# Optimization experiments

Hardware: AMD Instinct MI355X
Metric: run time of the kernel (lower is better)

## Reference

```python
import jax, jax.numpy as jnp
import numpy as np

N_ENC, IN_DIM, LATENT = 16, 256, 32
WIDTHS = [128, 64]
BATCH = 32768
NID_C = N_ENC * LATENT  # 512, identity width of the compressor


def _halving_widths():
    # halving_widths(n_encoders, 1) * n_encoders from the source
    ws, w = [], N_ENC
    while w >= 1:
        ws.append(N_ENC * w)
        w //= 2
    return ws  # [256, 128, 64, 32, 16]


def _residual_pairs(init_dim, final_dim):
    # (in, out) shapes of the linear layers inside the residual compressor/decompressor
    pairs, inp = [], 2 * init_dim  # DoublingBlock doubles the input first
    for o in _halving_widths():
        pairs.append((inp, o))
        inp = init_dim + o  # ResidualBlock output = identity (init_dim) + activated out
    pairs.append((inp, final_dim))
    return pairs


def setup_inputs() -> dict:
    key = jax.random.key(0)
    ks = iter(jax.random.split(key, 80))
    d = {}
    d["x"] = jax.random.normal(next(ks), (BATCH, N_ENC * IN_DIM), dtype=jnp.float32)
    enc_dims = [IN_DIM] + WIDTHS + [LATENT]
    for i in range(3):
        fi, fo = enc_dims[i], enc_dims[i + 1]
        d[f"enc_w{i}"] = jax.random.normal(next(ks), (N_ENC, fo, fi), dtype=jnp.float32) / np.float32(np.sqrt(fi))
        d[f"enc_b{i}"] = jnp.zeros((N_ENC, fo), dtype=jnp.float32)
    dec_dims = [LATENT] + WIDTHS[::-1] + [IN_DIM]
    for i in range(3):
        fi, fo = dec_dims[i], dec_dims[i + 1]
        d[f"dec_w{i}"] = jax.random.normal(next(ks), (N_ENC, fo, fi), dtype=jnp.float32) / np.float32(np.sqrt(fi))
        d[f"dec_b{i}"] = jnp.zeros((N_ENC, fo), dtype=jnp.float32)
    for i, (fi, fo) in enumerate(_residual_pairs(NID_C, LATENT)):
        d[f"comp_w{i}"] = jax.random.normal(next(ks), (fo, fi), dtype=jnp.float32) / np.float32(np.sqrt(fi))
        d[f"comp_b{i}"] = jnp.zeros((fo,), dtype=jnp.float32)
    for i, (fi, fo) in enumerate(_residual_pairs(LATENT, NID_C)):
        d[f"decomp_w{i}"] = jax.random.normal(next(ks), (fo, fi), dtype=jnp.float32) / np.float32(np.sqrt(fi))
        d[f"decomp_b{i}"] = jnp.zeros((fo,), dtype=jnp.float32)
    return d


def _stacked_mlp(h, ws, bs):
    # Block-diagonal stacked MLP: equivalent math to a dense Linear whose weight
    # is diagnolize_weights(per-model weights), expressed as a batched GEMM.
    B = h.shape[0]
    for i, (w, b) in enumerate(zip(ws, bs)):
        n, o, fi = w.shape
        h = jnp.einsum('bni,noi->bno', h.reshape(B, n, fi), w) + b  # b: (n, o)
        h = h.reshape(B, n * o)
        if i < len(ws) - 1:
            h = jax.nn.sigmoid(h)
    return h


def _residual_net(z, ws, bs, n_id):
    h = jnp.concatenate([z, z], axis=1)  # DoublingBlock
    for w, b in zip(ws[:-1], bs[:-1]):
        # ResidualBlock: concat(identity, act(Linear(full)))
        h = jnp.concatenate([h[:, :n_id], jax.nn.sigmoid(h @ w.T + b)], axis=1)
    return h @ ws[-1].T + bs[-1]


def reference(x, enc_w0, enc_b0, enc_w1, enc_b1, enc_w2, enc_b2,
              dec_w0, dec_b0, dec_w1, dec_b1, dec_w2, dec_b2,
              comp_w0, comp_b0, comp_w1, comp_b1, comp_w2, comp_b2,
              comp_w3, comp_b3, comp_w4, comp_b4, comp_w5, comp_b5,
              decomp_w0, decomp_b0, decomp_w1, decomp_b1, decomp_w2, decomp_b2,
              decomp_w3, decomp_b3, decomp_w4, decomp_b4, decomp_w5, decomp_b5):
    enc_ws = [enc_w0, enc_w1, enc_w2]; enc_bs = [enc_b0, enc_b1, enc_b2]
    dec_ws = [dec_w0, dec_w1, dec_w2]; dec_bs = [dec_b0, dec_b1, dec_b2]
    comp_ws = [comp_w0, comp_w1, comp_w2, comp_w3, comp_w4, comp_w5]
    comp_bs = [comp_b0, comp_b1, comp_b2, comp_b3, comp_b4, comp_b5]
    decomp_ws = [decomp_w0, decomp_w1, decomp_w2, decomp_w3, decomp_w4, decomp_w5]
    decomp_bs = [decomp_b0, decomp_b1, decomp_b2, decomp_b3, decomp_b4, decomp_b5]
    z_stack = _stacked_mlp(x, enc_ws, enc_bs)                 # (B, 512)
    z = _residual_net(z_stack, comp_ws, comp_bs, NID_C)       # (B, 32)
    z_stack_hat = _residual_net(z, decomp_ws, decomp_bs, LATENT)  # (B, 512)
    x_hat = _stacked_mlp(z_stack_hat, dec_ws, dec_bs)         # (B, 4096)
    return x_hat
```

## Files before the change

kernel.cpp:

```cpp
#include <hip/hip_runtime.h>

typedef __bf16 bf16x8 __attribute__((ext_vector_type(8)));
typedef __bf16 bf16x4 __attribute__((ext_vector_type(4)));
typedef float  f32x4  __attribute__((ext_vector_type(4)));

#define MFMA16(a, b, c) __builtin_amdgcn_mfma_f32_16x16x32_bf16((a), (b), (c), 0, 0, 0)

__device__ __forceinline__ float sigm(float x) { return 1.0f / (1.0f + __expf(-x)); }

enum : int {
  ENC_W0_OFF  = 0,
  ENC_W1_OFF  = 524288,
  ENC_W2_OFF  = 655360,
  DEC_W0_OFF  = 688128,
  DEC_W1_OFF  = 720896,
  DEC_W2_OFF  = 851968,
  COMP_W0_OFF = 1376256,
  COMP_W1_OFF = 1507328,
  COMP_W2_OFF = 1605632,
  COMP_W3_OFF = 1646592,
  COMP_W4_OFF = 1665024,
  COMP_W5_OFF = 1673728,
  DCMP_W0_OFF = 1691136,
  DCMP_W1_OFF = 1699328,
  DCMP_W2_OFF = 1736192,
  DCMP_W3_OFF = 1746432,
  DCMP_W4_OFF = 1749504,
  DCMP_W5_OFF = 1750528,
  W_TOTAL     = 1783296,
};

#define ZS_BYTES_OFF (4u * 1024u * 1024u)

__device__ __forceinline__ bf16x8 ldB(const __bf16* __restrict__ Wp, int nc16, int kf, int c, int lane) {
  return *(const bf16x8*)(Wp + (((size_t)(kf * nc16 + c)) * 64 + lane) * 8);
}

struct RC { int row, col; };
__device__ __forceinline__ RC unperm(int tl, int lg_nc16) {
  int frag = tl >> 9, ln = (tl >> 3) & 63, j = tl & 7;
  int kf = frag >> lg_nc16, c = frag & ((1 << lg_nc16) - 1);
  RC rc; rc.row = c * 16 + (ln & 15); rc.col = kf * 32 + ((ln >> 4) << 3) + j;
  return rc;
}

__global__ void prep_kernel(
    const float* __restrict__ ew0, const float* __restrict__ ew1, const float* __restrict__ ew2,
    const float* __restrict__ dw0, const float* __restrict__ dw1, const float* __restrict__ dw2,
    const float* __restrict__ cw0, const float* __restrict__ cw1, const float* __restrict__ cw2,
    const float* __restrict__ cw3, const float* __restrict__ cw4, const float* __restrict__ cw5,
    const float* __restrict__ xw0, const float* __restrict__ xw1, const float* __restrict__ xw2,
    const float* __restrict__ xw3, const float* __restrict__ xw4, const float* __restrict__ xw5,
    __bf16* __restrict__ wb)
{
  for (int i = blockIdx.x * blockDim.x + threadIdx.x; i < W_TOTAL; i += gridDim.x * blockDim.x) {
    float v;
    if (i < ENC_W1_OFF) {
      int t = i; int e = t >> 15; RC rc = unperm(t & 32767, 3);
      v = ew0[e * 32768 + rc.row * 256 + rc.col];
    } else if (i < ENC_W2_OFF) {
      int t = i - ENC_W1_OFF; int e = t >> 13; RC rc = unperm(t & 8191, 2);
      v = ew1[e * 8192 + rc.row * 128 + rc.col];
    } else if (i < DEC_W0_OFF) {
      int t = i - ENC_W2_OFF; int e = t >> 11; RC rc = unperm(t & 2047, 1);
      v = ew2[e * 2048 + rc.row * 64 + rc.col];
    } else if (i < DEC_W1_OFF) {
      int t = i - DEC_W0_OFF; int e = t >> 11; RC rc = unperm(t & 2047, 2);
      v = dw0[e * 2048 + rc.row * 32 + rc.col];
    } else if (i < DEC_W2_OFF) {
      int t = i - DEC_W1_OFF; int e = t >> 13; RC rc = unperm(t & 8191, 3);
      v = dw1[e * 8192 + rc.row * 64 + rc.col];
    } else if (i < COMP_W0_OFF) {
      int t = i - DEC_W2_OFF; int e = t >> 15; RC rc = unperm(t & 32767, 4);
      v = dw2[e * 32768 + rc.row * 128 + rc.col];
    } else if (i < COMP_W1_OFF) {
      RC rc = unperm(i - COMP_W0_OFF, 4);
      v = cw0[rc.row * 1024 + rc.col] + cw0[rc.row * 1024 + 512 + rc.col];
    } else if (i < COMP_W2_OFF) {
      RC rc = unperm(i - COMP_W1_OFF, 3); v = cw1[rc.row * 768 + rc.col];
    } else if (i < COMP_W3_OFF) {
      RC rc = unperm(i - COMP_W2_OFF, 2); v = cw2[rc.row * 640 + rc.col];
    } else if (i < COMP_W4_OFF) {
      RC rc = unperm(i - COMP_W3_OFF, 1); v = cw3[rc.row * 576 + rc.col];
    } else if (i < COMP_W5_OFF) {
      RC rc = unperm(i - COMP_W4_OFF, 0); v = cw4[rc.row * 544 + rc.col];
    } else if (i < DCMP_W0_OFF) {
      RC rc = unperm(i - COMP_W5_OFF, 1);
      v = (rc.col < 528) ? cw5[rc.row * 528 + rc.col] : 0.0f;
    } else if (i < DCMP_W1_OFF) {
      RC rc = unperm(i - DCMP_W0_OFF, 4);
      v = xw0[rc.row * 64 + rc.col] + xw0[rc.row * 64 + 32 + rc.col];
    } else if (i < DCMP_W2_OFF) {
      RC rc = unperm(i - DCMP_W1_OFF, 3); v = xw1[rc.row * 288 + rc.col];
    } else if (i < DCMP_W3_OFF) {
      RC rc = unperm(i - DCMP_W2_OFF, 2); v = xw2[rc.row * 160 + rc.col];
    } else if (i < DCMP_W4_OFF) {
      RC rc = unperm(i - DCMP_W3_OFF, 1); v = xw3[rc.row * 96 + rc.col];
    } else if (i < DCMP_W5_OFF) {
      RC rc = unperm(i - DCMP_W4_OFF, 0); v = xw4[rc.row * 64 + rc.col];
    } else {
      RC rc = unperm(i - DCMP_W5_OFF, 5);
      v = (rc.col < 48) ? xw5[rc.row * 48 + rc.col] : 0.0f;
    }
    wb[i] = (__bf16)v;
  }
}

__global__ __launch_bounds__(256, 3)
void enc_kernel(const float* __restrict__ x, const __bf16* __restrict__ wb,
                const float* __restrict__ b0, const float* __restrict__ b1,
                const float* __restrict__ b2, __bf16* __restrict__ zout)
{
  __shared__ __align__(16) char smem[51200];
  __bf16* xs = (__bf16*)smem;
  __bf16* h1 = (__bf16*)(smem + 33792);
  __bf16* h2 = (__bf16*)smem;
  const int e = blockIdx.x;
  const int m0 = blockIdx.y * 64;
  const int tid = threadIdx.x;
  const int lane = tid & 63, wv = tid >> 6;
  const int l15 = lane & 15, hi8 = (lane >> 4) * 8, rloc = (lane >> 4) * 4;

  const float* xblk = x + (size_t)m0 * 4096 + e * 256;
  #pragma unroll
  for (int i = 0; i < 16; ++i) {
    int idx = tid + i * 256;
    int r = idx >> 6, c4 = (idx & 63) * 4;
    float4 v = *(const float4*)(xblk + (size_t)r * 4096 + c4);
    bf16x4 o = { (__bf16)v.x, (__bf16)v.y, (__bf16)v.z, (__bf16)v.w };
    *(bf16x4*)&xs[r * 264 + c4] = o;
  }
  __syncthreads();

  {
    const __bf16* W = wb + ENC_W0_OFF + e * 32768;
    f32x4 acc[4][2];
    #pragma unroll
    for (int cf = 0; cf < 2; ++cf) {
      float bv = b0[e * 128 + wv * 32 + cf * 16 + l15];
      f32x4 bvv = {bv, bv, bv, bv};
      #pragma unroll
      for (int rf = 0; rf < 4; ++rf) acc[rf][cf] = bvv;
    }
    #pragma unroll
    for (int ks = 0; ks < 8; ++ks) {
      bf16x8 a[4], bb[2];
      #pragma unroll
      for (int rf = 0; rf < 4; ++rf) a[rf] = *(const bf16x8*)&xs[(rf * 16 + l15) * 264 + ks * 32 + hi8];
      #pragma unroll
      for (int cf = 0; cf < 2; ++cf) bb[cf] = ldB(W, 8, ks, wv * 2 + cf, lane);
      #pragma unroll
      for (int rf = 0; rf < 4; ++rf)
        #pragma unroll
        for (int cf = 0; cf < 2; ++cf)
          acc[rf][cf] = MFMA16(a[rf], bb[cf], acc[rf][cf]);
    }
    #pragma unroll
    for (int rf = 0; rf < 4; ++rf)
      #pragma unroll
      for (int cf = 0; cf < 2; ++cf)
        #pragma unroll
        for (int r = 0; r < 4; ++r)
          h1[(rf * 16 + rloc + r) * 136 + wv * 32 + cf * 16 + l15] = (__bf16)sigm(acc[rf][cf][r]);
  }
  __syncthreads();

  {
    const __bf16* W = wb + ENC_W1_OFF + e * 8192;
    f32x4 acc[4];
    float bv = b1[e * 64 + wv * 16 + l15];
    f32x4 bvv = {bv, bv, bv, bv};
    #pragma unroll
    for (int rf = 0; rf < 4; ++rf) acc[rf] = bvv;
    #pragma unroll
    for (int ks = 0; ks < 4; ++ks) {
      bf16x8 a[4];
      #pragma unroll
      for (int rf = 0; rf < 4; ++rf) a[rf] = *(const bf16x8*)&h1[(rf * 16 + l15) * 136 + ks * 32 + hi8];
      bf16x8 bb = ldB(W, 4, ks, wv, lane);
      #pragma unroll
      for (int rf = 0; rf < 4; ++rf) acc[rf] = MFMA16(a[rf], bb, acc[rf]);
    }
    #pragma unroll
    for (int rf = 0; rf < 4; ++rf)
      #pragma unroll
      for (int r = 0; r < 4; ++r)
        h2[(rf * 16 + rloc + r) * 72 + wv * 16 + l15] = (__bf16)sigm(acc[rf][r]);
  }
  __syncthreads();

  if (wv < 2) {
    const __bf16* W = wb + ENC_W2_OFF + e * 2048;
    f32x4 acc[4];
    float bv = b2[e * 32 + wv * 16 + l15];
    f32x4 bvv = {bv, bv, bv, bv};
    #pragma unroll
    for (int rf = 0; rf < 4; ++rf) acc[rf] = bvv;
    #pragma unroll
    for (int ks = 0; ks < 2; ++ks) {
      bf16x8 a[4];
      #pragma unroll
      for (int rf = 0; rf < 4; ++rf) a[rf] = *(const bf16x8*)&h2[(rf * 16 + l15) * 72 + ks * 32 + hi8];
      bf16x8 bb = ldB(W, 2, ks, wv, lane);
      #pragma unroll
      for (int rf = 0; rf < 4; ++rf) acc[rf] = MFMA16(a[rf], bb, acc[rf]);
    }
    #pragma unroll
    for (int rf = 0; rf < 4; ++rf)
      #pragma unroll
      for (int r = 0; r < 4; ++r)
        zout[(size_t)(m0 + rf * 16 + rloc + r) * 512 + e * 32 + wv * 16 + l15] = (__bf16)acc[rf][r];
  }
}

template<int NF, int KT, int ZKS, int ZLD, int SKS, int SLD, int DLD, bool SIG>
__device__ __forceinline__ void rlayer(const __bf16* __restrict__ W, const float* __restrict__ bias,
                                       const __bf16* __restrict__ zp, const __bf16* __restrict__ sp,
                                       __bf16* __restrict__ dst,
                                       int wv, int lane, int l15, int hi8, int rloc)
{
  constexpr int NJ = (NF >= 32) ? 4 : ((NF >= 16) ? 2 : 1);
  constexpr int NR = (NF >= 8) ? 4 : ((NF == 4) ? 2 : 1);
  int c0, row0;
  if constexpr (NF >= 8)       { c0 = wv;      row0 = 0; }
  else if constexpr (NF == 4)  { c0 = wv & 3;  row0 = (wv >> 2) * 32; }
  else if constexpr (NF == 2)  { c0 = wv & 1;  row0 = (wv >> 1) * 16; }
  else                         { if (wv >= 4) return; c0 = 0; row0 = wv * 16; }
  f32x4 acc[NR][NJ];
  #pragma unroll
  for (int j = 0; j < NJ; ++j) {
    float bv = bias[(c0 + 8 * j) * 16 + l15];
    f32x4 b4 = {bv, bv, bv, bv};
    #pragma unroll
    for (int rf = 0; rf < NR; ++rf) acc[rf][j] = b4;
  }
  #pragma unroll
  for (int ks = 0; ks < ZKS; ++ks) {
    bf16x8 a[NR];
    #pragma unroll
    for (int rf = 0; rf < NR; ++rf)
      a[rf] = *(const bf16x8*)&zp[(size_t)(row0 + rf * 16 + l15) * ZLD + ks * 32 + hi8];
    #pragma unroll
    for (int j = 0; j < NJ; ++j) {
      bf16x8 b = ldB(W, NF, ks, c0 + 8 * j, lane);
      #pragma unroll
      for (int rf = 0; rf < NR; ++rf) acc[rf][j] = MFMA16(a[rf], b, acc[rf][j]);
    }
  }
  if constexpr (SKS > 0) {
    #pragma unroll
    for (int ks = 0; ks < SKS; ++ks) {
      bf16x8 a[NR];
      #pragma unroll
      for (int rf = 0; rf < NR; ++rf)
        a[rf] = *(const bf16x8*)&sp[(size_t)(row0 + rf * 16 + l15) * SLD + ks * 32 + hi8];
      #pragma unroll
      for (int j = 0; j < NJ; ++j) {
        bf16x8 b = ldB(W, NF, ZKS + ks, c0 + 8 * j, lane);
        #pragma unroll
        for (int rf = 0; rf < NR; ++rf) acc[rf][j] = MFMA16(a[rf], b, acc[rf][j]);
      }
    }
  }
  #pragma unroll
  for (int j = 0; j < NJ; ++j)
    #pragma unroll
    for (int rf = 0; rf < NR; ++rf)
      #pragma unroll
      for (int r = 0; r < 4; ++r) {
        float v = acc[rf][j][r];
        dst[(size_t)(row0 + rf * 16 + rloc + r) * DLD + (c0 + 8 * j) * 16 + l15] =
            (__bf16)(SIG ? sigm(v) : v);
      }
}

struct MidBias {
  const float *c0, *c1, *c2, *c3, *c4, *c5;
  const float *x0, *x1, *x2, *x3, *x4, *x5;
};

__global__ __launch_bounds__(512, 2)
void mid_kernel(const __bf16* __restrict__ zin, const __bf16* __restrict__ wb,
                MidBias mb, __bf16* __restrict__ zhout)
{
  __shared__ __bf16 zs[64 * 520];
  __shared__ __bf16 sA[64 * 264];
  __shared__ __bf16 sB[64 * 136];
  __shared__ __bf16 zsm[64 * 40];
  const int tid = threadIdx.x;
  const int wv = tid >> 6, lane = tid & 63;
  const int l15 = lane & 15, hi8 = (lane >> 4) * 8, rloc = (lane >> 4) * 4;
  const int m0 = blockIdx.x * 64;

  #pragma unroll
  for (int i = 0; i < 8; ++i) {
    int idx = tid + i * 512;
    int r = idx >> 6, c8 = (idx & 63) * 8;
    *(bf16x8*)&zs[r * 520 + c8] = *(const bf16x8*)(zin + (size_t)(m0 + r) * 512 + c8);
  }
  __syncthreads();
  rlayer<16, 512, 16, 520, 0,   0, 264, true >(wb + COMP_W0_OFF, mb.c0, zs, nullptr, sA, wv, lane, l15, hi8, rloc); __syncthreads();
  rlayer< 8, 768, 16, 520, 8, 264, 136, true >(wb + COMP_W1_OFF, mb.c1, zs, sA, sB, wv, lane, l15, hi8, rloc); __syncthreads();
  rlayer< 4, 640, 16, 520, 4, 136, 264, true >(wb + COMP_W2_OFF, mb.c2, zs, sB, sA, wv, lane, l15, hi8, rloc); __syncthreads();
  rlayer< 2, 576, 16, 520, 2, 264, 136, true >(wb + COMP_W3_OFF, mb.c3, zs, sA, sB, wv, lane, l15, hi8, rloc); __syncthreads();
  rlayer< 1, 544, 16, 520, 1, 136, 264, true >(wb + COMP_W4_OFF, mb.c4, zs, sB, sA, wv, lane, l15, hi8, rloc);
  for (int i = tid; i < 64 * 16; i += 512) sA[(i >> 4) * 264 + 16 + (i & 15)] = (__bf16)0.0f;
  __syncthreads();
  rlayer< 2, 544, 16, 520, 1, 264, 40, false>(wb + COMP_W5_OFF, mb.c5, zs, sA, zsm, wv, lane, l15, hi8, rloc);
  __syncthreads();
  rlayer<16,  32, 1, 40, 0,   0, 264, true >(wb + DCMP_W0_OFF, mb.x0, zsm, nullptr, sA, wv, lane, l15, hi8, rloc); __syncthreads();
  rlayer< 8, 288, 1, 40, 8, 264, 136, true >(wb + DCMP_W1_OFF, mb.x1, zsm, sA, sB, wv, lane, l15, hi8, rloc); __syncthreads();
  rlayer< 4, 160, 1, 40, 4, 136, 264, true >(wb + DCMP_W2_OFF, mb.x2, zsm, sB, sA, wv, lane, l15, hi8, rloc); __syncthreads();
  rlayer< 2,  96, 1, 40, 2, 264, 136, true >(wb + DCMP_W3_OFF, mb.x3, zsm, sA, sB, wv, lane, l15, hi8, rloc); __syncthreads();
  rlayer< 1,  64, 1, 40, 1, 136, 264, true >(wb + DCMP_W4_OFF, mb.x4, zsm, sB, sA, wv, lane, l15, hi8, rloc);
  for (int i = tid; i < 64 * 16; i += 512) sA[(i >> 4) * 264 + 16 + (i & 15)] = (__bf16)0.0f;
  __syncthreads();
  rlayer<32,  64, 1, 40, 1, 264, 512, false>(wb + DCMP_W5_OFF, mb.x5, zsm, sA,
                                             zhout + (size_t)m0 * 512, wv, lane, l15, hi8, rloc);
}

__global__ __launch_bounds__(256, 4)
void dec_kernel(const __bf16* __restrict__ zin, const __bf16* __restrict__ wb,
                const float* __restrict__ b0, const float* __restrict__ b1,
                const float* __restrict__ b2, float* __restrict__ out)
{
  __shared__ __bf16 zs[64][40];
  __shared__ __bf16 h1[64][72];
  __shared__ __bf16 h2[64][136];
  const int e = blockIdx.x;
  const int m0 = blockIdx.y * 64;
  const int tid = threadIdx.x;
  const int lane = tid & 63, wv = tid >> 6;
  const int l15 = lane & 15, hi8 = (lane >> 4) * 8, rloc = (lane >> 4) * 4;

  {
    int r = tid >> 2, c = (tid & 3) * 8;
    *(bf16x8*)&zs[r][c] = *(const bf16x8*)(zin + (size_t)(m0 + r) * 512 + e * 32 + c);
  }
  __syncthreads();

  {
    const __bf16* W = wb + DEC_W0_OFF + e * 2048;
    f32x4 acc[4];
    float bv = b0[e * 64 + wv * 16 + l15];
    f32x4 bvv = {bv, bv, bv, bv};
    #pragma unroll
    for (int rf = 0; rf < 4; ++rf) acc[rf] = bvv;
    bf16x8 a[4];
    #pragma unroll
    for (int rf = 0; rf < 4; ++rf) a[rf] = *(const bf16x8*)&zs[rf * 16 + l15][hi8];
    bf16x8 bb = ldB(W, 4, 0, wv, lane);
    #pragma unroll
    for (int rf = 0; rf < 4; ++rf) acc[rf] = MFMA16(a[rf], bb, acc[rf]);
    #pragma unroll
    for (int rf = 0; rf < 4; ++rf)
      #pragma unroll
      for (int r = 0; r < 4; ++r)
        h1[rf * 16 + rloc + r][wv * 16 + l15] = (__bf16)sigm(acc[rf][r]);
  }
  __syncthreads();

  {
    const __bf16* W = wb + DEC_W1_OFF + e * 8192;
    f32x4 acc[4][2];
    #pragma unroll
    for (int cf = 0; cf < 2; ++cf) {
      float bv = b1[e * 128 + wv * 32 + cf * 16 + l15];
      f32x4 bvv = {bv, bv, bv, bv};
      #pragma unroll
      for (int rf = 0; rf < 4; ++rf) acc[rf][cf] = bvv;
    }
    #pragma unroll
    for (int ks = 0; ks < 2; ++ks) {
      bf16x8 a[4], bb[2];
      #pragma unroll
      for (int rf = 0; rf < 4; ++rf) a[rf] = *(const bf16x8*)&h1[rf * 16 + l15][ks * 32 + hi8];
      #pragma unroll
      for (int cf = 0; cf < 2; ++cf) bb[cf] = ldB(W, 8, ks, wv * 2 + cf, lane);
      #pragma unroll
      for (int rf = 0; rf < 4; ++rf)
        #pragma unroll
        for (int cf = 0; cf < 2; ++cf)
          acc[rf][cf] = MFMA16(a[rf], bb[cf], acc[rf][cf]);
    }
    #pragma unroll
    for (int rf = 0; rf < 4; ++rf)
      #pragma unroll
      for (int cf = 0; cf < 2; ++cf)
        #pragma unroll
        for (int r = 0; r < 4; ++r)
          h2[rf * 16 + rloc + r][wv * 32 + cf * 16 + l15] = (__bf16)sigm(acc[rf][cf][r]);
  }
  __syncthreads();

  {
    const __bf16* W = wb + DEC_W2_OFF + e * 32768;
    f32x4 acc[4][4];
    #pragma unroll
    for (int cf = 0; cf < 4; ++cf) {
      float bv = b2[e * 256 + wv * 64 + cf * 16 + l15];
      f32x4 bvv = {bv, bv, bv, bv};
      #pragma unroll
      for (int rf = 0; rf < 4; ++rf) acc[rf][cf] = bvv;
    }
    #pragma unroll
    for (int ks = 0; ks < 4; ++ks) {
      bf16x8 a[4], bb[4];
      #pragma unroll
      for (int rf = 0; rf < 4; ++rf) a[rf] = *(const bf16x8*)&h2[rf * 16 + l15][ks * 32 + hi8];
      #pragma unroll
      for (int cf = 0; cf < 4; ++cf) bb[cf] = ldB(W, 16, ks, wv * 4 + cf, lane);
      #pragma unroll
      for (int rf = 0; rf < 4; ++rf)
        #pragma unroll
        for (int cf = 0; cf < 4; ++cf)
          acc[rf][cf] = MFMA16(a[rf], bb[cf], acc[rf][cf]);
    }
    #pragma unroll
    for (int rf = 0; rf < 4; ++rf)
      #pragma unroll
      for (int cf = 0; cf < 4; ++cf)
        #pragma unroll
        for (int r = 0; r < 4; ++r)
          out[(size_t)(m0 + rf * 16 + rloc + r) * 4096 + e * 256 + wv * 64 + cf * 16 + l15] =
              acc[rf][cf][r];
  }
}

extern "C" void kernel_launch(void* const* d_in, const int* in_sizes, int n_in,
                              void* d_out, int out_size, void* d_ws, size_t ws_size,
                              hipStream_t stream) {
  (void)in_sizes; (void)n_in; (void)out_size; (void)ws_size;
  const float* x   = (const float*)d_in[0];
  const float* ew0 = (const float*)d_in[1];  const float* eb0 = (const float*)d_in[2];
  const float* ew1 = (const float*)d_in[3];  const float* eb1 = (const float*)d_in[4];
  const float* ew2 = (const float*)d_in[5];  const float* eb2 = (const float*)d_in[6];
  const float* dw0 = (const float*)d_in[7];  const float* db0 = (const float*)d_in[8];
  const float* dw1 = (const float*)d_in[9];  const float* db1 = (const float*)d_in[10];
  const float* dw2 = (const float*)d_in[11]; const float* db2 = (const float*)d_in[12];
  const float* cw[6]; const float* cb[6];
  for (int i = 0; i < 6; ++i) { cw[i] = (const float*)d_in[13 + 2 * i]; cb[i] = (const float*)d_in[14 + 2 * i]; }
  const float* xw[6]; const float* xb[6];
  for (int i = 0; i < 6; ++i) { xw[i] = (const float*)d_in[25 + 2 * i]; xb[i] = (const float*)d_in[26 + 2 * i]; }

  __bf16* wbuf   = (__bf16*)d_ws;
  __bf16* zstack = (__bf16*)((char*)d_ws + ZS_BYTES_OFF);
  float* out = (float*)d_out;

  prep_kernel<<<1024, 256, 0, stream>>>(ew0, ew1, ew2, dw0, dw1, dw2,
                                        cw[0], cw[1], cw[2], cw[3], cw[4], cw[5],
                                        xw[0], xw[1], xw[2], xw[3], xw[4], xw[5], wbuf);
  enc_kernel<<<dim3(16, 512), 256, 0, stream>>>(x, wbuf, eb0, eb1, eb2, zstack);
  MidBias mb = {cb[0], cb[1], cb[2], cb[3], cb[4], cb[5],
                xb[0], xb[1], xb[2], xb[3], xb[4], xb[5]};
  mid_kernel<<<512, 512, 0, stream>>>(zstack, wbuf, mb, zstack);
  dec_kernel<<<dim3(16, 512), 256, 0, stream>>>(zstack, wbuf, db0, db1, db2, out);
}
```

Baseline: 345.3 us.

## Double encoder block to 512 threads and redistribute MFMA tiles across eight waves

The encoder kernel now launches 512 threads per block instead of 256, with launch bounds raised to allow up to six blocks per CU. Each of the eight waves takes a narrower slice of every layer: one 16-column fragment in layer 0, a 16x32 sub-tile in layer 1, and a single 16x16 tile in layer 2, so all waves stay busy in the last layer where half of them were idle before. The aim is more latency hiding and better use of the CU during the memory-heavy x load. In exchange each wave gets less register reuse of the A fragments, LDS read traffic per MFMA goes up, and the tighter launch bounds may cap registers per thread.

```diff
diff --git a/kernel.cpp b/kernel.cpp
--- a/kernel.cpp
+++ b/kernel.cpp
@@ -106,7 +106,7 @@
   }
 }
 
-__global__ __launch_bounds__(256, 3)
+__global__ __launch_bounds__(512, 6)
 void enc_kernel(const float* __restrict__ x, const __bf16* __restrict__ wb,
                 const float* __restrict__ b0, const float* __restrict__ b1,
                 const float* __restrict__ b2, __bf16* __restrict__ zout)
@@ -123,8 +123,8 @@
 
   const float* xblk = x + (size_t)m0 * 4096 + e * 256;
   #pragma unroll
-  for (int i = 0; i < 16; ++i) {
-    int idx = tid + i * 256;
+  for (int i = 0; i < 8; ++i) {
+    int idx = tid + i * 512;
     int r = idx >> 6, c4 = (idx & 63) * 4;
     float4 v = *(const float4*)(xblk + (size_t)r * 4096 + c4);
     bf16x4 o = { (__bf16)v.x, (__bf16)v.y, (__bf16)v.z, (__bf16)v.w };
@@ -134,82 +134,66 @@
 
   {
     const __bf16* W = wb + ENC_W0_OFF + e * 32768;
-    f32x4 acc[4][2];
-    #pragma unroll
-    for (int cf = 0; cf < 2; ++cf) {
-      float bv = b0[e * 128 + wv * 32 + cf * 16 + l15];
-      f32x4 bvv = {bv, bv, bv, bv};
-      #pragma unroll
-      for (int rf = 0; rf < 4; ++rf) acc[rf][cf] = bvv;
-    }
+    f32x4 acc[4];
+    float bv = b0[e * 128 + wv * 16 + l15];
+    f32x4 bvv = {bv, bv, bv, bv};
+    #pragma unroll
+    for (int rf = 0; rf < 4; ++rf) acc[rf] = bvv;
     #pragma unroll
     for (int ks = 0; ks < 8; ++ks) {
-      bf16x8 a[4], bb[2];
-      #pragma unroll
-      for (int rf = 0; rf < 4; ++rf) a[rf] = *(const bf16x8*)&xs[(rf * 16 + l15) * 264 + ks * 32 + hi8];
-      #pragma unroll
-      for (int cf = 0; cf < 2; ++cf) bb[cf] = ldB(W, 8, ks, wv * 2 + cf, lane);
-      #pragma unroll
-      for (int rf = 0; rf < 4; ++rf)
-        #pragma unroll
-        for (int cf = 0; cf < 2; ++cf)
-          acc[rf][cf] = MFMA16(a[rf], bb[cf], acc[rf][cf]);
+      bf16x8 bb = ldB(W, 8, ks, wv, lane);
+      #pragma unroll
+      for (int rf = 0; rf < 4; ++rf) {
+        bf16x8 a = *(const bf16x8*)&xs[(rf * 16 + l15) * 264 + ks * 32 + hi8];
+        acc[rf] = MFMA16(a, bb, acc[rf]);
+      }
     }
     #pragma unroll
     for (int rf = 0; rf < 4; ++rf)
       #pragma unroll
-      for (int cf = 0; cf < 2; ++cf)
-        #pragma unroll
-        for (int r = 0; r < 4; ++r)
-          h1[(rf * 16 + rloc + r) * 136 + wv * 32 + cf * 16 + l15] = (__bf16)sigm(acc[rf][cf][r]);
+      for (int r = 0; r < 4; ++r)
+        h1[(rf * 16 + rloc + r) * 136 + wv * 16 + l15] = (__bf16)sigm(acc[rf][r]);
   }
   __syncthreads();
 
   {
     const __bf16* W = wb + ENC_W1_OFF + e * 8192;
-    f32x4 acc[4];
-    float bv = b1[e * 64 + wv * 16 + l15];
+    const int wc = wv & 3, wr = wv >> 2;
+    f32x4 acc[2];
+    float bv = b1[e * 64 + wc * 16 + l15];
     f32x4 bvv = {bv, bv, bv, bv};
-    #pragma unroll
-    for (int rf = 0; rf < 4; ++rf) acc[rf] = bvv;
+    acc[0] = bvv; acc[1] = bvv;
     #pragma unroll
     for (int ks = 0; ks < 4; ++ks) {
-      bf16x8 a[4];
-      #pragma unroll
-      for (int rf = 0; rf < 4; ++rf) a[rf] = *(const bf16x8*)&h1[(rf * 16 + l15) * 136 + ks * 32 + hi8];
-      bf16x8 bb = ldB(W, 4, ks, wv, lane);
-      #pragma unroll
-      for (int rf = 0; rf < 4; ++rf) acc[rf] = MFMA16(a[rf], bb, acc[rf]);
-    }
-    #pragma unroll
-    for (int rf = 0; rf < 4; ++rf)
+      bf16x8 bb = ldB(W, 4, ks, wc, lane);
+      #pragma unroll
+      for (int rf = 0; rf < 2; ++rf) {
+        bf16x8 a = *(const bf16x8*)&h1[(wr * 32 + rf * 16 + l15) * 136 + ks * 32 + hi8];
+        acc[rf] = MFMA16(a, bb, acc[rf]);
+      }
+    }
+    #pragma unroll
+    for (int rf = 0; rf < 2; ++rf)
       #pragma unroll
       for (int r = 0; r < 4; ++r)
-        h2[(rf * 16 + rloc + r) * 72 + wv * 16 + l15] = (__bf16)sigm(acc[rf][r]);
-  }
-  __syncthreads();
-
-  if (wv < 2) {
+        h2[(wr * 32 + rf * 16 + rloc + r) * 72 + wc * 16 + l15] = (__bf16)sigm(acc[rf][r]);
+  }
+  __syncthreads();
+
+  {
     const __bf16* W = wb + ENC_W2_OFF + e * 2048;
-    f32x4 acc[4];
-    float bv = b2[e * 32 + wv * 16 + l15];
-    f32x4 bvv = {bv, bv, bv, bv};
-    #pragma unroll
-    for (int rf = 0; rf < 4; ++rf) acc[rf] = bvv;
+    const int wc2 = wv & 1, wq = wv >> 1;
+    float bv = b2[e * 32 + wc2 * 16 + l15];
+    f32x4 acc = {bv, bv, bv, bv};
     #pragma unroll
     for (int ks = 0; ks < 2; ++ks) {
-      bf16x8 a[4];
-      #pragma unroll
-      for (int rf = 0; rf < 4; ++rf) a[rf] = *(const bf16x8*)&h2[(rf * 16 + l15) * 72 + ks * 32 + hi8];
-      bf16x8 bb = ldB(W, 2, ks, wv, lane);
-      #pragma unroll
-      for (int rf = 0; rf < 4; ++rf) acc[rf] = MFMA16(a[rf], bb, acc[rf]);
-    }
-    #pragma unroll
-    for (int rf = 0; rf < 4; ++rf)
-      #pragma unroll
-      for (int r = 0; r < 4; ++r)
-        zout[(size_t)(m0 + rf * 16 + rloc + r) * 512 + e * 32 + wv * 16 + l15] = (__bf16)acc[rf][r];
+      bf16x8 a = *(const bf16x8*)&h2[(wq * 16 + l15) * 72 + ks * 32 + hi8];
+      bf16x8 bb = ldB(W, 2, ks, wc2, lane);
+      acc = MFMA16(a, bb, acc);
+    }
+    #pragma unroll
+    for (int r = 0; r < 4; ++r)
+      zout[(size_t)(m0 + wq * 16 + rloc + r) * 512 + e * 32 + wc2 * 16 + l15] = (__bf16)acc[r];
   }
 }
 
@@ -450,7 +434,7 @@
   prep_kernel<<<1024, 256, 0, stream>>>(ew0, ew1, ew2, dw0, dw1, dw2,
                                         cw[0], cw[1], cw[2], cw[3], cw[4], cw[5],
                                         xw[0], xw[1], xw[2], xw[3], xw[4], xw[5], wbuf);
-  enc_kernel<<<dim3(16, 512), 256, 0, stream>>>(x, wbuf, eb0, eb1, eb2, zstack);
+  enc_kernel<<<dim3(16, 512), 512, 0, stream>>>(x, wbuf, eb0, eb1, eb2, zstack);
   MidBias mb = {cb[0], cb[1], cb[2], cb[3], cb[4], cb[5],
                 xb[0], xb[1], xb[2], xb[3], xb[4], xb[5]};
   mid_kernel<<<512, 512, 0, stream>>>(zstack, wbuf, mb, zstack);
```

Result: no change. 346.8 us (+0.5%).
